# Performance work log

Hardware: AMD Instinct MI355X
Metric: run time of the kernel (lower is better)

Reference implementation:

```python
import jax, jax.numpy as jnp
import numpy as np

N_ATOMS = 100000
N_EDGES = 200000  # paired: edge 2i and 2i+1 are reverses of each other
N_MOLS = 4096
D_V, D_E, D_H = 133, 14, 512
DEPTH = 3
BN_EPS = 1e-5


def setup_inputs() -> dict:
    key = jax.random.key(0)
    ks = jax.random.split(key, 10)
    V = jax.random.normal(ks[0], (N_ATOMS, D_V), dtype=jnp.float32)
    E = jax.random.normal(ks[1], (N_EDGES, D_E), dtype=jnp.float32)
    # paired directed edges: (src,dst) at 2i, (dst,src) at 2i+1 -> rev index is i^1
    half = N_EDGES // 2
    s = jax.random.randint(ks[2], (half,), 0, N_ATOMS, dtype=jnp.int32)
    d = jax.random.randint(ks[3], (half,), 0, N_ATOMS, dtype=jnp.int32)
    edge_src = jnp.stack([s, d], axis=1).reshape(-1)
    edge_dst = jnp.stack([d, s], axis=1).reshape(-1)
    batch = jnp.sort(jax.random.randint(ks[4], (N_ATOMS,), 0, N_MOLS, dtype=jnp.int32))
    sc = 0.02
    W_i = jax.random.normal(ks[5], (D_V + D_E, D_H), dtype=jnp.float32) * sc
    W_h = jax.random.normal(ks[6], (D_H, D_H), dtype=jnp.float32) * sc
    W_o = jax.random.normal(ks[7], (D_V + D_H, D_H), dtype=jnp.float32) * sc
    b_o = jnp.zeros((D_H,), dtype=jnp.float32)
    gamma = jnp.ones((D_H,), dtype=jnp.float32)
    beta = jnp.zeros((D_H,), dtype=jnp.float32)
    return {"V": V, "E": E, "edge_src": edge_src, "edge_dst": edge_dst,
            "batch": batch, "W_i": W_i, "W_h": W_h, "W_o": W_o, "b_o": b_o,
            "gamma": gamma, "beta": beta}


def reference(V, E, edge_src, edge_dst, batch, W_i, W_h, W_o, b_o, gamma, beta):
    n_atoms = V.shape[0]
    n_edges = E.shape[0]
    rev = jnp.arange(n_edges, dtype=jnp.int32) ^ 1  # reverse-bond index

    # --- BondMessagePassing (chemprop v2) ---
    # initialize: H_0 = W_i([V[src] ; E]), H = relu(H_0)
    H0 = jnp.concatenate([V[edge_src], E], axis=1) @ W_i  # [n_edges, d_h]
    H = jax.nn.relu(H0)
    for _ in range(DEPTH - 1):
        # message: sum of incoming edge states at dst node, gathered at src,
        # minus the reverse edge's own state
        M_node = jax.ops.segment_sum(H, edge_dst, num_segments=n_atoms)
        M = M_node[edge_src] - H[rev]
        # update: H = relu(H_0 + W_h(M)) (dropout = 0)
        H = jax.nn.relu(H0 + M @ W_h)
    # finalize: aggregate edges to nodes, H_v = relu(W_o([V ; M_v]))
    M_v = jax.ops.segment_sum(H, edge_dst, num_segments=n_atoms)
    H_v = jax.nn.relu(jnp.concatenate([V, M_v], axis=1) @ W_o + b_o)  # [n_atoms, d_h]

    # --- MeanAggregation over batch ids ---
    sums = jax.ops.segment_sum(H_v, batch, num_segments=N_MOLS)
    counts = jax.ops.segment_sum(jnp.ones((n_atoms,), H_v.dtype), batch, num_segments=N_MOLS)
    h_mol = sums / jnp.maximum(counts, 1.0)[:, None]  # [n_mols, d_h]

    # --- BatchNorm1d (training mode: batch statistics, biased variance) ---
    mu = h_mol.mean(axis=0)
    var = h_mol.var(axis=0)
    return (h_mol - mu) * jax.lax.rsqrt(var + BN_EPS) * gamma + beta
```

## Files before the change

kernel.cpp:

```cpp
#include <hip/hip_runtime.h>

typedef _Float16 f16;
typedef _Float16 half8 __attribute__((ext_vector_type(8)));
typedef _Float16 half4v __attribute__((ext_vector_type(4)));
typedef float f32x4 __attribute__((ext_vector_type(4)));

#define N_ATOMS 100000
#define N_EDGES 200000
#define N_MOLS  4096
#define D_V 133
#define D_E 14
#define D_H 512
#define KC  672
#define KSE 21
#define LDA 40

__global__ void wt_build_swz(const float* __restrict__ W1, int r1,
                             const float* __restrict__ W2, int r2,
                             f16* __restrict__ WtS) {
    int gid = blockIdx.x * blockDim.x + threadIdx.x;
    if (gid >= D_H * KC) return;
    int n = gid / KC;
    int k = gid - n * KC;
    float x = 0.f;
    if (k < r1) x = W1[k * D_H + n];
    else if (k < r1 + r2) x = W2[(k - r1) * D_H + n];
    const int dst = ((((n >> 4) * KSE + (k >> 5)) << 6) + (((k >> 3) & 3) << 4) + (n & 15)) * 8 + (k & 7);
    WtS[dst] = (f16)x;
}

__global__ void csr_hist(const int* __restrict__ edst, int* __restrict__ cnt) {
    int e = blockIdx.x * blockDim.x + threadIdx.x;
    if (e < N_EDGES) atomicAdd(&cnt[edst[e]], 1);
}

__global__ __launch_bounds__(1024) void csr_scan(const int* __restrict__ cnt,
                                                 int* __restrict__ off, int* __restrict__ pos) {
    __shared__ int sums[1024];
    const int tid = threadIdx.x;
    const int lo = tid * 100;
    int s = 0;
    if (lo < N_ATOMS) {
        const int4* c4 = reinterpret_cast<const int4*>(cnt + lo);
        #pragma unroll
        for (int i = 0; i < 25; ++i) { int4 v = c4[i]; s += v.x + v.y + v.z + v.w; }
    }
    sums[tid] = s;
    __syncthreads();
    for (int d = 1; d < 1024; d <<= 1) {
        int v = (tid >= d) ? sums[tid - d] : 0;
        __syncthreads();
        sums[tid] += v;
        __syncthreads();
    }
    int run = sums[tid] - s;
    if (lo < N_ATOMS) {
        const int4* c4 = reinterpret_cast<const int4*>(cnt + lo);
        for (int i = 0; i < 25; ++i) {
            int4 v = c4[i];
            const int b = lo + i * 4;
            off[b]     = run; pos[b]     = run; run += v.x;
            off[b + 1] = run; pos[b + 1] = run; run += v.y;
            off[b + 2] = run; pos[b + 2] = run; run += v.z;
            off[b + 3] = run; pos[b + 3] = run; run += v.w;
        }
    }
    if (tid == 1023) off[N_ATOMS] = run;
}

__global__ void csr_scatter(const int* __restrict__ edst, int* __restrict__ pos,
                            int* __restrict__ eid) {
    int e = blockIdx.x * blockDim.x + threadIdx.x;
    if (e < N_EDGES) {
        int idx = atomicAdd(&pos[edst[e]], 1);
        eid[idx] = e;
    }
}

template<bool F16M>
__global__ __launch_bounds__(512) void seg_csr(
    const f16* __restrict__ H, const int* __restrict__ off, const int* __restrict__ eid,
    void* __restrict__ MnOut, float* __restrict__ Msc)
{
    const int n = blockIdx.x * 8 + (threadIdx.x >> 6);
    const int lane = threadIdx.x & 63;
    const int j0 = off[n], j1 = off[n + 1];
    float acc[8];
    #pragma unroll
    for (int k = 0; k < 8; ++k) acc[k] = 0.f;
    int e_cur = (j0 < j1) ? eid[j0] : 0;
    for (int j = j0; j < j1; ++j) {
        const int e_nxt = (j + 1 < j1) ? eid[j + 1] : 0;
        const half8 h = *reinterpret_cast<const half8*>(&H[e_cur * D_H + lane * 8]);
        #pragma unroll
        for (int k = 0; k < 8; ++k) acc[k] += (float)h[k];
        e_cur = e_nxt;
    }
    if (F16M) {
        half8 o;
        #pragma unroll
        for (int k = 0; k < 8; ++k) o[k] = (f16)acc[k];
        *reinterpret_cast<half8*>(&((f16*)MnOut)[n * D_H + lane * 8]) = o;
    } else {
        float m = 0.f;
        #pragma unroll
        for (int k = 0; k < 8; ++k) m = fmaxf(m, fabsf(acc[k]));
        m = fmaxf(m, __shfl_xor(m, 1));
        m = fmaxf(m, __shfl_xor(m, 2));
        m = fmaxf(m, 1e-20f);
        const float s = m * (1.f / 127.f);
        const float inv_s = 127.f / m;
        if ((lane & 3) == 0) Msc[n * 16 + (lane >> 2)] = s;
        int q[8];
        #pragma unroll
        for (int k = 0; k < 8; ++k) q[k] = __float2int_rn(acc[k] * inv_s);
        uint2 o;
        o.x = (q[0] & 0xff) | ((q[1] & 0xff) << 8) | ((q[2] & 0xff) << 16) | ((unsigned)(q[3] & 0xff) << 24);
        o.y = (q[4] & 0xff) | ((q[5] & 0xff) << 8) | ((q[6] & 0xff) << 16) | ((unsigned)(q[7] & 0xff) << 24);
        *reinterpret_cast<uint2*>(&((unsigned int*)MnOut)[n * 128 + lane * 2]) = o;
    }
}

template<bool F16M>
__global__ __launch_bounds__(512) void gemm_pass(
    const float* __restrict__ V, const float* __restrict__ E,
    const int* __restrict__ esrc, const void* __restrict__ Mn,
    const float* __restrict__ Msc,
    f16* __restrict__ Ha, const f16* __restrict__ WtS, int ks_begin)
{
    __shared__ __align__(16) f16 Al[64 * LDA];
    const int tid = threadIdx.x;
    const int rowblk = blockIdx.x << 6;
    const int srow = tid >> 3;
    const int skk  = (tid & 7) << 2;
    const int e_s  = rowblk + srow;
    const int sv   = esrc[e_s];
    const int rev  = e_s ^ 1;
    const int lane = tid & 63;
    const int quad = lane >> 4;
    const int m16  = lane & 15;
    const int colbase = (tid >> 6) << 6;
    const int cb0 = (tid >> 6) << 2;
    const f16* WtL = WtS + lane * 8;

    f32x4 acc[4][4];
    #pragma unroll
    for (int a = 0; a < 4; ++a)
    #pragma unroll
    for (int b = 0; b < 4; ++b)
    #pragma unroll
    for (int r = 0; r < 4; ++r) acc[a][b][r] = 0.f;

    char4 pq; float ps; half4v pm; half4v ph; float pv[4];
    auto issue = [&](int ks) {
        const int k0 = ks << 5;
        if (k0 < D_H) {
            if (F16M) {
                pm = *reinterpret_cast<const half4v*>(&((const f16*)Mn)[sv * D_H + k0 + skk]);
            } else {
                pq = *reinterpret_cast<const char4*>(&((const char*)Mn)[sv * D_H + k0 + skk]);
                ps = Msc[sv * 16 + (k0 >> 5)];
            }
            ph = *reinterpret_cast<const half4v*>(&Ha[rev * D_H + k0 + skk]);
        } else {
            #pragma unroll
            for (int j = 0; j < 4; ++j) {
                const int kk = k0 + skk + j - D_H;
                float x = 0.f;
                if (kk < D_V) x = V[sv * D_V + kk];
                else if (kk < D_V + D_E) x = E[e_s * D_E + (kk - D_V)];
                pv[j] = x;
            }
        }
    };

    issue(ks_begin);
    for (int ks = ks_begin; ks < KSE; ++ks) {
        const int k0 = ks << 5;
        half4v w;
        if (k0 < D_H) {
            if (F16M) {
                w = pm - ph;
            } else {
                w[0] = (f16)((float)pq.x * ps - (float)ph[0]);
                w[1] = (f16)((float)pq.y * ps - (float)ph[1]);
                w[2] = (f16)((float)pq.z * ps - (float)ph[2]);
                w[3] = (f16)((float)pq.w * ps - (float)ph[3]);
            }
        } else {
            w[0] = (f16)pv[0]; w[1] = (f16)pv[1]; w[2] = (f16)pv[2]; w[3] = (f16)pv[3];
        }
        __syncthreads();
        *reinterpret_cast<half4v*>(&Al[srow * LDA + skk]) = w;
        __syncthreads();
        if (ks + 1 < KSE) issue(ks + 1);
        half8 af[4];
        #pragma unroll
        for (int rt = 0; rt < 4; ++rt)
            af[rt] = *reinterpret_cast<const half8*>(&Al[(rt * 16 + m16) * LDA + quad * 8]);
        #pragma unroll
        for (int ct = 0; ct < 4; ++ct) {
            const half8 bf = *reinterpret_cast<const half8*>(&WtL[(((cb0 + ct) * KSE + ks) << 9)]);
            #pragma unroll
            for (int rt = 0; rt < 4; ++rt)
                acc[rt][ct] = __builtin_amdgcn_mfma_f32_16x16x32_f16(af[rt], bf, acc[rt][ct], 0, 0, 0);
        }
    }

    #pragma unroll
    for (int rt = 0; rt < 4; ++rt)
    #pragma unroll
    for (int ct = 0; ct < 4; ++ct)
    #pragma unroll
    for (int r = 0; r < 4; ++r) {
        const int row = rowblk + rt * 16 + quad * 4 + r;
        const int col = colbase + ct * 16 + m16;
        Ha[row * D_H + col] = (f16)fmaxf(acc[rt][ct][r], 0.f);
    }
}

template<bool F16M>
__global__ __launch_bounds__(512) void gemm_out(
    const float* __restrict__ V, const void* __restrict__ Mn,
    const float* __restrict__ Msc, const float* __restrict__ bo,
    const f16* __restrict__ WtS, f16* __restrict__ Hv)
{
    __shared__ __align__(16) f16 Al[2][64 * LDA];
    __shared__ float bo_s[D_H];
    const int tid = threadIdx.x;
    const int rowblk = blockIdx.x << 6;
    bo_s[tid] = bo[tid];
    const int srow = tid >> 3;
    const int skk  = (tid & 7) << 2;
    const int arow = min(rowblk + srow, N_ATOMS - 1);
    const int lane = tid & 63;
    const int quad = lane >> 4;
    const int m16  = lane & 15;
    const int colbase = (tid >> 6) << 6;
    const int cb0 = (tid >> 6) << 2;
    const f16* WtL = WtS + lane * 8;

    f32x4 acc[4][4];
    #pragma unroll
    for (int a = 0; a < 4; ++a)
    #pragma unroll
    for (int b = 0; b < 4; ++b)
    #pragma unroll
    for (int r = 0; r < 4; ++r) acc[a][b][r] = 0.f;

    char4 pq0, pq1; float ps0, ps1;
    half4v pm0, pm1;
    float pv0[4], pv1[4];

#define GO_ISSUE(S, KSV) do {                                                        \
    const int ks_i_ = (KSV);                                                         \
    if (ks_i_ < KSE) {                                                               \
        const int k0_ = ks_i_ << 5;                                                  \
        if (k0_ < D_H) {                                                             \
            if (F16M) {                                                              \
                pm##S = *reinterpret_cast<const half4v*>(&((const f16*)Mn)[arow * D_H + k0_ + skk]); \
            } else {                                                                 \
                pq##S = *reinterpret_cast<const char4*>(&((const char*)Mn)[arow * D_H + k0_ + skk]); \
                ps##S = Msc[arow * 16 + (k0_ >> 5)];                                 \
            }                                                                        \
        } else {                                                                     \
            const int kb_ = k0_ + skk - D_H;                                         \
            pv##S[0] = (kb_ + 0 < D_V) ? V[arow * D_V + kb_ + 0] : 0.f;              \
            pv##S[1] = (kb_ + 1 < D_V) ? V[arow * D_V + kb_ + 1] : 0.f;              \
            pv##S[2] = (kb_ + 2 < D_V) ? V[arow * D_V + kb_ + 2] : 0.f;              \
            pv##S[3] = (kb_ + 3 < D_V) ? V[arow * D_V + kb_ + 3] : 0.f;              \
        }                                                                            \
    }                                                                                \
} while (0)

#define GO_MAKEW(S, KSV, W) do {                                                     \
    const int k0_ = (KSV) << 5;                                                      \
    if (k0_ < D_H) {                                                                 \
        if (F16M) { W = pm##S; }                                                     \
        else {                                                                       \
            W[0] = (f16)((float)pq##S.x * ps##S);                                    \
            W[1] = (f16)((float)pq##S.y * ps##S);                                    \
            W[2] = (f16)((float)pq##S.z * ps##S);                                    \
            W[3] = (f16)((float)pq##S.w * ps##S);                                    \
        }                                                                            \
    } else {                                                                         \
        W[0] = (f16)pv##S[0]; W[1] = (f16)pv##S[1];                                  \
        W[2] = (f16)pv##S[2]; W[3] = (f16)pv##S[3];                                  \
    }                                                                                \
} while (0)

#define GO_MFMA(KSV, CUR) do {                                                       \
    half8 af[4];                                                                     \
    _Pragma("unroll")                                                                \
    for (int rt = 0; rt < 4; ++rt)                                                   \
        af[rt] = *reinterpret_cast<const half8*>(&Al[CUR][(rt * 16 + m16) * LDA + quad * 8]); \
    _Pragma("unroll")                                                                \
    for (int ct = 0; ct < 4; ++ct) {                                                 \
        const half8 bf = *reinterpret_cast<const half8*>(&WtL[(((cb0 + ct) * KSE + (KSV)) << 9)]); \
        _Pragma("unroll")                                                            \
        for (int rt = 0; rt < 4; ++rt)                                               \
            acc[rt][ct] = __builtin_amdgcn_mfma_f32_16x16x32_f16(af[rt], bf, acc[rt][ct], 0, 0, 0); \
    }                                                                                \
} while (0)

    GO_ISSUE(0, 0);
    GO_ISSUE(1, 1);
    {
        half4v w;
        GO_MAKEW(0, 0, w);
        *reinterpret_cast<half4v*>(&Al[0][srow * LDA + skk]) = w;
        GO_ISSUE(0, 2);
    }
    __syncthreads();

    #pragma unroll 2
    for (int i = 0; i < KSE - 1; ++i) {
        const int ks = i;
        const int cur = i & 1;
        {
            half4v w;
            if ((i + 1) & 1) { GO_MAKEW(1, ks + 1, w); }
            else             { GO_MAKEW(0, ks + 1, w); }
            *reinterpret_cast<half4v*>(&Al[cur ^ 1][srow * LDA + skk]) = w;
            if ((i + 1) & 1) { GO_ISSUE(1, ks + 3); }
            else             { GO_ISSUE(0, ks + 3); }
        }
        GO_MFMA(ks, cur);
        __syncthreads();
    }
    GO_MFMA(KSE - 1, (KSE - 1) & 1);

#undef GO_ISSUE
#undef GO_MAKEW
#undef GO_MFMA

    #pragma unroll
    for (int rt = 0; rt < 4; ++rt)
    #pragma unroll
    for (int ct = 0; ct < 4; ++ct)
    #pragma unroll
    for (int r = 0; r < 4; ++r) {
        const int row = rowblk + rt * 16 + quad * 4 + r;
        if (row < N_ATOMS) {
            const int col = colbase + ct * 16 + m16;
            Hv[row * D_H + col] = (f16)fmaxf(acc[rt][ct][r] + bo_s[col], 0.f);
        }
    }
}

__global__ __launch_bounds__(512) void mol_mean(
    const f16* __restrict__ Hv, const int* __restrict__ batch, float* __restrict__ mean)
{
    const int m = blockIdx.x;
    __shared__ int sh[2];
    if (threadIdx.x == 0) {
        int lo = 0, hi = N_ATOMS;
        while (lo < hi) { int mid = (lo + hi) >> 1; if (batch[mid] < m) lo = mid + 1; else hi = mid; }
        sh[0] = lo;
        int lo2 = lo; hi = N_ATOMS;
        while (lo2 < hi) { int mid = (lo2 + hi) >> 1; if (batch[mid] < m + 1) lo2 = mid + 1; else hi = mid; }
        sh[1] = lo2;
    }
    __syncthreads();
    const int a0 = sh[0], a1 = sh[1];
    float acc = 0.f;
    for (int a = a0; a < a1; ++a) acc += (float)Hv[(size_t)a * D_H + threadIdx.x];
    mean[m * D_H + threadIdx.x] = acc / (float)max(a1 - a0, 1);
}

__global__ __launch_bounds__(256) void bn_stats(
    const float* __restrict__ mean_in, const float* __restrict__ gamma,
    const float* __restrict__ beta, float* __restrict__ An, float* __restrict__ Bn)
{
    const int n = blockIdx.x;
    const int tid = threadIdx.x;
    float s = 0.f, s2 = 0.f;
    for (int m = tid; m < N_MOLS; m += 256) {
        float h = mean_in[m * D_H + n];
        s += h; s2 += h * h;
    }
    for (int off = 32; off > 0; off >>= 1) {
        s  += __shfl_down(s, off);
        s2 += __shfl_down(s2, off);
    }
    __shared__ float sh[8];
    const int wave = tid >> 6, lane = tid & 63;
    if (lane == 0) { sh[wave] = s; sh[4 + wave] = s2; }
    __syncthreads();
    if (tid == 0) {
        float S  = sh[0] + sh[1] + sh[2] + sh[3];
        float S2 = sh[4] + sh[5] + sh[6] + sh[7];
        float mu = S / (float)N_MOLS;
        float var = fmaxf(S2 / (float)N_MOLS - mu * mu, 0.f);
        float sc = rsqrtf(var + 1e-5f) * gamma[n];
        An[n] = sc;
        Bn[n] = beta[n] - mu * sc;
    }
}

__global__ void bn_apply(const float* __restrict__ mean_in,
                         const float* __restrict__ An, const float* __restrict__ Bn,
                         float* __restrict__ out)
{
    int gid = blockIdx.x * blockDim.x + threadIdx.x;
    int n = gid & 511;
    out[gid] = mean_in[gid] * An[n] + Bn[n];
}

extern "C" void kernel_launch(void* const* d_in, const int* in_sizes, int n_in,
                              void* d_out, int out_size, void* d_ws, size_t ws_size,
                              hipStream_t stream)
{
    (void)in_sizes; (void)n_in; (void)out_size;
    const float* V     = (const float*)d_in[0];
    const float* E     = (const float*)d_in[1];
    const int*   esrc  = (const int*)d_in[2];
    const int*   edst  = (const int*)d_in[3];
    const int*   batch = (const int*)d_in[4];
    const float* Wi    = (const float*)d_in[5];
    const float* Wh    = (const float*)d_in[6];
    const float* Wo    = (const float*)d_in[7];
    const float* bo    = (const float*)d_in[8];
    const float* gam   = (const float*)d_in[9];
    const float* bet   = (const float*)d_in[10];
    float* out = (float*)d_out;

    char* ws = (char*)d_ws;
    f16*   WtC  = (f16*)(ws + 0);
    f16*   WtO  = (f16*)(ws + 688128);
    int*   off  = (int*)(ws + 1376256);
    int*   eid  = (int*)(ws + 1776384);
    int*   cnt  = (int*)(ws + 2576384);
    float* An   = (float*)(ws + 2992768);
    float* Bn   = (float*)(ws + 2994816);
    f16*   Ha   = (f16*)(ws + 2996864);
    void*  Mn   = (void*)(ws + 207796864);
    float* Msc  = (float*)(ws + 258996864);
    f16*   Hv   = Ha;
    float* mean = out;

    const bool f16m = ws_size >= 310196864ULL;

    wt_build_swz<<<(D_H * KC + 255) / 256, 256, 0, stream>>>(Wh, D_H, Wi, D_V + D_E, WtC);
    wt_build_swz<<<(D_H * KC + 255) / 256, 256, 0, stream>>>(Wo + D_V * D_H, D_H, Wo, D_V, WtO);

    hipMemsetAsync(cnt, 0, 400000, stream);
    csr_hist<<<(N_EDGES + 511) / 512, 512, 0, stream>>>(edst, cnt);
    csr_scan<<<1, 1024, 0, stream>>>(cnt, off, cnt);
    csr_scatter<<<(N_EDGES + 511) / 512, 512, 0, stream>>>(edst, cnt, eid);

    if (f16m) {
        gemm_pass<true><<<N_EDGES / 64, 512, 0, stream>>>(V, E, esrc, Mn, Msc, Ha, WtC, 16);
        for (int it = 0; it < 2; ++it) {
            seg_csr<true><<<N_ATOMS / 8, 512, 0, stream>>>(Ha, off, eid, Mn, Msc);
            gemm_pass<true><<<N_EDGES / 64, 512, 0, stream>>>(V, E, esrc, Mn, Msc, Ha, WtC, 0);
        }
        seg_csr<true><<<N_ATOMS / 8, 512, 0, stream>>>(Ha, off, eid, Mn, Msc);
        gemm_out<true><<<(N_ATOMS + 63) / 64, 512, 0, stream>>>(V, Mn, Msc, bo, WtO, Hv);
    } else {
        gemm_pass<false><<<N_EDGES / 64, 512, 0, stream>>>(V, E, esrc, Mn, Msc, Ha, WtC, 16);
        for (int it = 0; it < 2; ++it) {
            seg_csr<false><<<N_ATOMS / 8, 512, 0, stream>>>(Ha, off, eid, Mn, Msc);
            gemm_pass<false><<<N_EDGES / 64, 512, 0, stream>>>(V, E, esrc, Mn, Msc, Ha, WtC, 0);
        }
        seg_csr<false><<<N_ATOMS / 8, 512, 0, stream>>>(Ha, off, eid, Mn, Msc);
        gemm_out<false><<<(N_ATOMS + 63) / 64, 512, 0, stream>>>(V, Mn, Msc, bo, WtO, Hv);
    }

    mol_mean<<<N_MOLS, 512, 0, stream>>>(Hv, batch, mean);
    bn_stats<<<D_H, 256, 0, stream>>>(mean, gam, bet, An, Bn);
    bn_apply<<<(N_MOLS * D_H) / 256, 256, 0, stream>>>(mean, An, Bn, out);
}
```

Before: 1.251 ms.

## Double-buffer LDS A tile in gemm_pass with one barrier per k-step

Converts the edge GEMM pass to a double-buffered shared-memory A tile. The next k-slice is formed and stored into the alternate buffer while the current MFMAs run, and global loads are issued two steps ahead. This removes one of the two __syncthreads per k-step and overlaps gather/convert work with matrix math. It also makes the start k-step a template parameter and adds launch_bounds(512,4), which may constrain registers and cause spills given the 64-float accumulator set.

```diff
diff --git a/kernel.cpp b/kernel.cpp
--- a/kernel.cpp
+++ b/kernel.cpp
@@ -121,14 +121,14 @@
     }
 }
 
-template<bool F16M>
-__global__ __launch_bounds__(512) void gemm_pass(
+template<bool F16M, int KS0>
+__global__ __launch_bounds__(512, 4) void gemm_pass(
     const float* __restrict__ V, const float* __restrict__ E,
     const int* __restrict__ esrc, const void* __restrict__ Mn,
     const float* __restrict__ Msc,
-    f16* __restrict__ Ha, const f16* __restrict__ WtS, int ks_begin)
-{
-    __shared__ __align__(16) f16 Al[64 * LDA];
+    f16* __restrict__ Ha, const f16* __restrict__ WtS)
+{
+    __shared__ __align__(16) f16 Al[2 * 64 * LDA];
     const int tid = threadIdx.x;
     const int rowblk = blockIdx.x << 6;
     const int srow = tid >> 3;
@@ -173,9 +173,7 @@
             }
         }
     };
-
-    issue(ks_begin);
-    for (int ks = ks_begin; ks < KSE; ++ks) {
+    auto makew = [&](int ks) -> half4v {
         const int k0 = ks << 5;
         half4v w;
         if (k0 < D_H) {
@@ -190,14 +188,30 @@
         } else {
             w[0] = (f16)pv[0]; w[1] = (f16)pv[1]; w[2] = (f16)pv[2]; w[3] = (f16)pv[3];
         }
-        __syncthreads();
+        return w;
+    };
+
+    issue(KS0);
+    {
+        half4v w = makew(KS0);
         *reinterpret_cast<half4v*>(&Al[srow * LDA + skk]) = w;
-        __syncthreads();
-        if (ks + 1 < KSE) issue(ks + 1);
+    }
+    issue(KS0 + 1);
+    asm volatile("s_waitcnt lgkmcnt(0)" ::: "memory");
+    __builtin_amdgcn_sched_barrier(0);
+    __builtin_amdgcn_s_barrier();
+
+    int lso = 0;
+    for (int ks = KS0; ks < KSE; ++ks) {
         half8 af[4];
         #pragma unroll
         for (int rt = 0; rt < 4; ++rt)
-            af[rt] = *reinterpret_cast<const half8*>(&Al[(rt * 16 + m16) * LDA + quad * 8]);
+            af[rt] = *reinterpret_cast<const half8*>(&Al[lso + (rt * 16 + m16) * LDA + quad * 8]);
+        if (ks + 1 < KSE) {
+            half4v w = makew(ks + 1);
+            *reinterpret_cast<half4v*>(&Al[(lso ^ (64 * LDA)) + srow * LDA + skk]) = w;
+            if (ks + 2 < KSE) issue(ks + 2);
+        }
         #pragma unroll
         for (int ct = 0; ct < 4; ++ct) {
             const half8 bf = *reinterpret_cast<const half8*>(&WtL[(((cb0 + ct) * KSE + ks) << 9)]);
@@ -205,6 +219,10 @@
             for (int rt = 0; rt < 4; ++rt)
                 acc[rt][ct] = __builtin_amdgcn_mfma_f32_16x16x32_f16(af[rt], bf, acc[rt][ct], 0, 0, 0);
         }
+        asm volatile("s_waitcnt lgkmcnt(0)" ::: "memory");
+        __builtin_amdgcn_sched_barrier(0);
+        __builtin_amdgcn_s_barrier();
+        lso ^= (64 * LDA);
     }
 
     #pragma unroll
@@ -450,18 +468,18 @@
     csr_scatter<<<(N_EDGES + 511) / 512, 512, 0, stream>>>(edst, cnt, eid);
 
     if (f16m) {
-        gemm_pass<true><<<N_EDGES / 64, 512, 0, stream>>>(V, E, esrc, Mn, Msc, Ha, WtC, 16);
+        gemm_pass<true, 16><<<N_EDGES / 64, 512, 0, stream>>>(V, E, esrc, Mn, Msc, Ha, WtC);
         for (int it = 0; it < 2; ++it) {
             seg_csr<true><<<N_ATOMS / 8, 512, 0, stream>>>(Ha, off, eid, Mn, Msc);
-            gemm_pass<true><<<N_EDGES / 64, 512, 0, stream>>>(V, E, esrc, Mn, Msc, Ha, WtC, 0);
+            gemm_pass<true, 0><<<N_EDGES / 64, 512, 0, stream>>>(V, E, esrc, Mn, Msc, Ha, WtC);
         }
         seg_csr<true><<<N_ATOMS / 8, 512, 0, stream>>>(Ha, off, eid, Mn, Msc);
         gemm_out<true><<<(N_ATOMS + 63) / 64, 512, 0, stream>>>(V, Mn, Msc, bo, WtO, Hv);
     } else {
-        gemm_pass<false><<<N_EDGES / 64, 512, 0, stream>>>(V, E, esrc, Mn, Msc, Ha, WtC, 16);
+        gemm_pass<false, 16><<<N_EDGES / 64, 512, 0, stream>>>(V, E, esrc, Mn, Msc, Ha, WtC);
         for (int it = 0; it < 2; ++it) {
             seg_csr<false><<<N_ATOMS / 8, 512, 0, stream>>>(Ha, off, eid, Mn, Msc);
-            gemm_pass<false><<<N_EDGES / 64, 512, 0, stream>>>(V, E, esrc, Mn, Msc, Ha, WtC, 0);
+            gemm_pass<false, 0><<<N_EDGES / 64, 512, 0, stream>>>(V, E, esrc, Mn, Msc, Ha, WtC);
         }
         seg_csr<false><<<N_ATOMS / 8, 512, 0, stream>>>(Ha, off, eid, Mn, Msc);
         gemm_out<false><<<(N_ATOMS + 63) / 64, 512, 0, stream>>>(V, Mn, Msc, bo, WtO, Hv);
```

New measurement: 1.405 ms. 12.3% more time.

## Shrink gemm_pass tile to 16 rows with 64-wide K steps and 256 threads

Applied to the files above, without the earlier changes.

Restructures the edge GEMM so each block handles 16 edge rows with 4 waves covering 128 columns each, staging 64-wide K chunks in shared memory. The grid grows fourfold and launch bounds target higher occupancy. The aim is more parallelism and fewer barriers per K. The cost is that weight fragments get reused across only 16 rows, which raises weight reads from L2 fourfold.

```diff
diff --git a/kernel.cpp b/kernel.cpp
--- a/kernel.cpp
+++ b/kernel.cpp
@@ -13,7 +13,9 @@
 #define D_H 512
 #define KC  672
 #define KSE 21
+#define KSE64 11
 #define LDA 40
+#define LDA64 72
 
 __global__ void wt_build_swz(const float* __restrict__ W1, int r1,
                              const float* __restrict__ W2, int r2,
@@ -122,44 +124,42 @@
 }
 
 template<bool F16M>
-__global__ __launch_bounds__(512) void gemm_pass(
+__global__ __launch_bounds__(256, 5) void gemm_pass(
     const float* __restrict__ V, const float* __restrict__ E,
     const int* __restrict__ esrc, const void* __restrict__ Mn,
     const float* __restrict__ Msc,
     f16* __restrict__ Ha, const f16* __restrict__ WtS, int ks_begin)
 {
-    __shared__ __align__(16) f16 Al[64 * LDA];
+    __shared__ __align__(16) f16 Al[16 * LDA64];
     const int tid = threadIdx.x;
-    const int rowblk = blockIdx.x << 6;
-    const int srow = tid >> 3;
-    const int skk  = (tid & 7) << 2;
+    const int rowblk = blockIdx.x << 4;
+    const int srow = tid >> 4;
+    const int skk  = (tid & 15) << 2;
     const int e_s  = rowblk + srow;
     const int sv   = esrc[e_s];
     const int rev  = e_s ^ 1;
     const int lane = tid & 63;
     const int quad = lane >> 4;
     const int m16  = lane & 15;
-    const int colbase = (tid >> 6) << 6;
-    const int cb0 = (tid >> 6) << 2;
+    const int colbase = (tid >> 6) << 7;
+    const int cb0 = (tid >> 6) << 3;
     const f16* WtL = WtS + lane * 8;
 
-    f32x4 acc[4][4];
-    #pragma unroll
-    for (int a = 0; a < 4; ++a)
-    #pragma unroll
-    for (int b = 0; b < 4; ++b)
-    #pragma unroll
-    for (int r = 0; r < 4; ++r) acc[a][b][r] = 0.f;
+    f32x4 acc[8];
+    #pragma unroll
+    for (int b = 0; b < 8; ++b)
+    #pragma unroll
+    for (int r = 0; r < 4; ++r) acc[b][r] = 0.f;
 
     char4 pq; float ps; half4v pm; half4v ph; float pv[4];
     auto issue = [&](int ks) {
-        const int k0 = ks << 5;
+        const int k0 = ks << 6;
         if (k0 < D_H) {
             if (F16M) {
                 pm = *reinterpret_cast<const half4v*>(&((const f16*)Mn)[sv * D_H + k0 + skk]);
             } else {
                 pq = *reinterpret_cast<const char4*>(&((const char*)Mn)[sv * D_H + k0 + skk]);
-                ps = Msc[sv * 16 + (k0 >> 5)];
+                ps = Msc[sv * 16 + ((k0 + skk) >> 5)];
             }
             ph = *reinterpret_cast<const half4v*>(&Ha[rev * D_H + k0 + skk]);
         } else {
@@ -175,8 +175,8 @@
     };
 
     issue(ks_begin);
-    for (int ks = ks_begin; ks < KSE; ++ks) {
-        const int k0 = ks << 5;
+    for (int ks = ks_begin; ks < KSE64; ++ks) {
+        const int k0 = ks << 6;
         half4v w;
         if (k0 < D_H) {
             if (F16M) {
@@ -191,31 +191,30 @@
             w[0] = (f16)pv[0]; w[1] = (f16)pv[1]; w[2] = (f16)pv[2]; w[3] = (f16)pv[3];
         }
         __syncthreads();
-        *reinterpret_cast<half4v*>(&Al[srow * LDA + skk]) = w;
+        *reinterpret_cast<half4v*>(&Al[srow * LDA64 + skk]) = w;
         __syncthreads();
-        if (ks + 1 < KSE) issue(ks + 1);
-        half8 af[4];
-        #pragma unroll
-        for (int rt = 0; rt < 4; ++rt)
-            af[rt] = *reinterpret_cast<const half8*>(&Al[(rt * 16 + m16) * LDA + quad * 8]);
-        #pragma unroll
-        for (int ct = 0; ct < 4; ++ct) {
-            const half8 bf = *reinterpret_cast<const half8*>(&WtL[(((cb0 + ct) * KSE + ks) << 9)]);
-            #pragma unroll
-            for (int rt = 0; rt < 4; ++rt)
-                acc[rt][ct] = __builtin_amdgcn_mfma_f32_16x16x32_f16(af[rt], bf, acc[rt][ct], 0, 0, 0);
-        }
-    }
-
-    #pragma unroll
-    for (int rt = 0; rt < 4; ++rt)
-    #pragma unroll
-    for (int ct = 0; ct < 4; ++ct)
+        if (ks + 1 < KSE64) issue(ks + 1);
+        #pragma unroll
+        for (int kk = 0; kk < 2; ++kk) {
+            const int ks32 = ks * 2 + kk;
+            if (ks32 < KSE) {
+                const half8 af = *reinterpret_cast<const half8*>(&Al[m16 * LDA64 + kk * 32 + quad * 8]);
+                #pragma unroll
+                for (int ct = 0; ct < 8; ++ct) {
+                    const half8 bf = *reinterpret_cast<const half8*>(&WtL[(((cb0 + ct) * KSE + ks32) << 9)]);
+                    acc[ct] = __builtin_amdgcn_mfma_f32_16x16x32_f16(af, bf, acc[ct], 0, 0, 0);
+                }
+            }
+        }
+    }
+
+    #pragma unroll
+    for (int ct = 0; ct < 8; ++ct)
     #pragma unroll
     for (int r = 0; r < 4; ++r) {
-        const int row = rowblk + rt * 16 + quad * 4 + r;
+        const int row = rowblk + quad * 4 + r;
         const int col = colbase + ct * 16 + m16;
-        Ha[row * D_H + col] = (f16)fmaxf(acc[rt][ct][r], 0.f);
+        Ha[row * D_H + col] = (f16)fmaxf(acc[ct][r], 0.f);
     }
 }
 
@@ -450,18 +449,18 @@
     csr_scatter<<<(N_EDGES + 511) / 512, 512, 0, stream>>>(edst, cnt, eid);
 
     if (f16m) {
-        gemm_pass<true><<<N_EDGES / 64, 512, 0, stream>>>(V, E, esrc, Mn, Msc, Ha, WtC, 16);
+        gemm_pass<true><<<N_EDGES / 16, 256, 0, stream>>>(V, E, esrc, Mn, Msc, Ha, WtC, 8);
         for (int it = 0; it < 2; ++it) {
             seg_csr<true><<<N_ATOMS / 8, 512, 0, stream>>>(Ha, off, eid, Mn, Msc);
-            gemm_pass<true><<<N_EDGES / 64, 512, 0, stream>>>(V, E, esrc, Mn, Msc, Ha, WtC, 0);
+            gemm_pass<true><<<N_EDGES / 16, 256, 0, stream>>>(V, E, esrc, Mn, Msc, Ha, WtC, 0);
         }
         seg_csr<true><<<N_ATOMS / 8, 512, 0, stream>>>(Ha, off, eid, Mn, Msc);
         gemm_out<true><<<(N_ATOMS + 63) / 64, 512, 0, stream>>>(V, Mn, Msc, bo, WtO, Hv);
     } else {
-        gemm_pass<false><<<N_EDGES / 64, 512, 0, stream>>>(V, E, esrc, Mn, Msc, Ha, WtC, 16);
+        gemm_pass<false><<<N_EDGES / 16, 256, 0, stream>>>(V, E, esrc, Mn, Msc, Ha, WtC, 8);
         for (int it = 0; it < 2; ++it) {
             seg_csr<false><<<N_ATOMS / 8, 512, 0, stream>>>(Ha, off, eid, Mn, Msc);
-            gemm_pass<false><<<N_EDGES / 64, 512, 0, stream>>>(V, E, esrc, Mn, Msc, Ha, WtC, 0);
+            gemm_pass<false><<<N_EDGES / 16, 256, 0, stream>>>(V, E, esrc, Mn, Msc, Ha, WtC, 0);
         }
         seg_csr<false><<<N_ATOMS / 8, 512, 0, stream>>>(Ha, off, eid, Mn, Msc);
         gemm_out<false><<<(N_ATOMS + 63) / 64, 512, 0, stream>>>(V, Mn, Msc, bo, WtO, Hv);
```

After: 1.578 ms. +26.1%, slower.
